# Optimization experiments

Hardware: AMD Instinct MI355X
Metric: run time of the kernel (lower is better)

The kernel has to match this reference:

```python
import jax, jax.numpy as jnp
import numpy as np

HEADS, DIM_HEAD, K_NN, EMB = 4, 64, 16, 256
INNER = HEADS * DIM_HEAD  # 256
POS_HID = 64
ATTN_HID = 4 * DIM_HEAD  # per-head hidden of grouped 1x1 conv MLP


def setup_inputs() -> dict:
    key = jax.random.key(0)
    ks = jax.random.split(key, 16)
    b, n = 2, 4096
    s = 0.05
    inp = {
        "x": jax.random.normal(ks[0], (b, n, EMB), jnp.float32),
        "mask": jnp.ones((b, n), dtype=bool),
        "pos": jax.random.normal(ks[1], (b, n, 3), jnp.float32),
        # to_qkv (no bias)
        "Wqkv": jax.random.normal(ks[2], (EMB, 3 * INNER), jnp.float32) * s,
        # pos_mlp: Linear(3,64) -> ReLU -> Linear(64, inner)
        "Wp1": jax.random.normal(ks[3], (3, POS_HID), jnp.float32) * s,
        "bp1": jax.random.normal(ks[4], (POS_HID,), jnp.float32) * s,
        "Wp2": jax.random.normal(ks[5], (POS_HID, INNER), jnp.float32) * s,
        "bp2": jax.random.normal(ks[6], (INNER,), jnp.float32) * s,
        # attn_mlp: grouped 1x1 convs == per-head linears [h, d_in, d_out]
        "Wa1": jax.random.normal(ks[7], (HEADS, DIM_HEAD, ATTN_HID), jnp.float32) * s,
        "ba1": jax.random.normal(ks[8], (HEADS, ATTN_HID), jnp.float32) * s,
        "Wa2": jax.random.normal(ks[9], (HEADS, ATTN_HID, DIM_HEAD), jnp.float32) * s,
        "ba2": jax.random.normal(ks[10], (HEADS, DIM_HEAD), jnp.float32) * s,
        # to_out
        "Wo": jax.random.normal(ks[11], (INNER, EMB), jnp.float32) * s,
        "bo": jax.random.normal(ks[12], (EMB,), jnp.float32) * s,
    }
    return inp


def reference(x, mask, pos, Wqkv, Wp1, bp1, Wp2, bp2, Wa1, ba1, Wa2, ba2, Wo, bo):
    b, n, _ = x.shape
    h, dh = HEADS, DIM_HEAD

    qkv = x @ Wqkv                              # [b, n, 3*inner]
    q, k, v = jnp.split(qkv, 3, axis=-1)
    to_heads = lambda t: t.reshape(b, n, h, dh).transpose(0, 2, 1, 3)  # [b,h,n,d]
    q, k, v = to_heads(q), to_heads(k), to_heads(v)

    # kNN on pos (per batch, squared euclidean, includes self)
    sq = jnp.sum(pos * pos, axis=-1)
    d2 = sq[:, :, None] + sq[:, None, :] - 2.0 * jnp.einsum('bid,bjd->bij', pos, pos)
    idx = jax.lax.top_k(-d2, K_NN)[1]            # [b, n, K]

    gat_h = jax.vmap(lambda t, i: t[:, i])       # [h,n,d],[n,K] -> [h,n,K,d]
    gat = jax.vmap(lambda t, i: t[i])            # [n,c],[n,K]  -> [n,K,c]

    qg = gat_h(q, idx)                           # [b,h,n,K,d]
    kg = gat_h(k, idx)
    vg = gat_h(v, idx)

    rel = gat(pos, idx) - pos[:, :, None, :]     # [b,n,K,3]
    rpe = jax.nn.relu(rel @ Wp1 + bp1) @ Wp2 + bp2               # [b,n,K,inner]
    rpe = rpe.reshape(b, n, K_NN, h, dh).transpose(0, 3, 1, 2, 4)  # [b,h,n,K,d]

    attn_in = qg - kg + rpe                      # [b,h,n,K,d]
    hid = jax.nn.relu(jnp.einsum('bhnkd,hde->bhnke', attn_in, Wa1)
                      + ba1[None, :, None, None, :])
    sim = (jnp.einsum('bhnke,hed->bhnkd', hid, Wa2)
           + ba2[None, :, None, None, :])        # [b,h,n,K,d]

    mg = jax.vmap(lambda m, i: m[i])(mask, idx)  # [b,n,K]
    pair = (mask[:, :, None] & mg)[:, None, :, :, None]
    sim = jnp.where(pair, sim, -jnp.finfo(sim.dtype).max)

    attn = jax.nn.softmax(sim, axis=3)           # over neighbors j
    # F.normalize over dim=-2 of [b,(h d),i,j] == over the point axis i
    attn = attn / jnp.maximum(jnp.linalg.norm(attn, axis=2, keepdims=True), 1e-12)

    agg = jnp.sum(attn * (vg + rpe), axis=3)     # [b,h,n,d]
    agg = agg.transpose(0, 2, 1, 3).reshape(b, n, h * dh)
    return agg @ Wo + bo
```

## Files before the change

### kernel.cpp

```cpp
#include <hip/hip_runtime.h>
#include <float.h>

typedef unsigned int uint;
typedef unsigned short ushort;

typedef _Float16 f16x8 __attribute__((ext_vector_type(8)));
typedef float f32x4 __attribute__((ext_vector_type(4)));
#define MFMA_F16(A, B, C) __builtin_amdgcn_mfma_f32_16x16x32_f16(A, B, C, 0, 0, 0)

__device__ __forceinline__ ushort f2h(float f) {
    _Float16 h = (_Float16)f;
    return __builtin_bit_cast(ushort, h);
}
__device__ __forceinline__ float h2f(ushort u) {
    _Float16 h = __builtin_bit_cast(_Float16, u);
    return (float)h;
}
__device__ __forceinline__ uint pack2(float a, float b) {
    return (uint)f2h(a) | ((uint)f2h(b) << 16);
}
__device__ __forceinline__ uint pkrtz(float a, float b) {
    return __builtin_bit_cast(uint, __builtin_amdgcn_cvt_pkrtz(a, b));
}
__device__ __forceinline__ f16x8 cast8(uint4 u) {
    return __builtin_bit_cast(f16x8, u);
}

template <int CTRL>
__device__ __forceinline__ void dpp_min(float& v, int& j) {
    int vp = __builtin_amdgcn_update_dpp(__float_as_int(v), __float_as_int(v),
                                         CTRL, 0xF, 0xF, false);
    int jp = __builtin_amdgcn_update_dpp(j, j, CTRL, 0xF, 0xF, false);
    float vf = __int_as_float(vp);
    bool better = (vf < v) || (vf == v && jp < j);
    v = better ? vf : v;
    j = better ? jp : j;
}
__device__ __forceinline__ void wave_min(float& v, int& j) {
    dpp_min<0x121>(v, j);
    dpp_min<0x122>(v, j);
    dpp_min<0x124>(v, j);
    dpp_min<0x128>(v, j);
    float ov = __shfl_xor(v, 16);
    int oj = __shfl_xor(j, 16);
    bool better = (ov < v) || (ov == v && oj < j);
    v = better ? ov : v;
    j = better ? oj : j;
    ov = __shfl_xor(v, 32);
    oj = __shfl_xor(j, 32);
    better = (ov < v) || (ov == v && oj < j);
    v = better ? ov : v;
    j = better ? oj : j;
}

__global__ void prep_kernel(const float* __restrict__ Wqkv, const float* __restrict__ Wa1,
                            const float* __restrict__ Wa2, const float* __restrict__ Wo,
                            const float* __restrict__ Wp2, const float* __restrict__ ba1,
                            ushort* __restrict__ WcatT, ushort* __restrict__ Wa1T,
                            ushort* __restrict__ Wa2T, ushort* __restrict__ WoT,
                            ushort* __restrict__ Wp2T, ushort* __restrict__ ba1p) {
    int t = blockIdx.x * 256 + threadIdx.x;
    {
        int cc2 = t >> 8, kk = t & 255;
        float val;
        if (cc2 < 256) val = Wqkv[kk * 768 + cc2] - Wqkv[kk * 768 + 256 + cc2];
        else           val = Wqkv[kk * 768 + 256 + cc2];
        WcatT[t] = f2h(val);
    }
    if (t < 65536) {
        int hh = t >> 14, r = t & 16383;
        int e = r >> 6, kin = r & 63;
        Wa1T[t] = f2h(Wa1[((size_t)(hh * 64 + kin)) * 256 + e]);
        int d = r >> 8, pos = r & 255;
        int ec = pos >> 5, lg = (pos >> 3) & 3, q = pos & 7;
        int e2 = ec * 32 + ((q >> 2) & 1) * 16 + lg * 4 + (q & 3);
        Wa2T[t] = f2h(Wa2[((size_t)(hh * 256 + e2)) * 64 + d]);
        int c3 = t >> 8, k3 = t & 255;
        WoT[t] = f2h(Wo[k3 * 256 + c3]);
    }
    if (t < 16384) {
        int row = t >> 6, p = t & 63;
        int h = row >> 6, s = row & 63;
        int ct = s >> 4, rr = s & 15;
        int d = (ct >> 1) * 32 + ((rr >> 2) & 3) * 8 + (ct & 1) * 4 + (rr & 3);
        Wp2T[t] = f2h(Wp2[p * 256 + h * 64 + d]);
    }
    if (t < 1024) {
        int h = t >> 8, pos = t & 255;
        int ec = pos >> 5, lg = (pos >> 3) & 3, q = pos & 7;
        int e2 = ec * 32 + ((q >> 2) & 1) * 16 + lg * 4 + (q & 3);
        ba1p[t] = f2h(ba1[h * 256 + e2]);
    }
}

__global__ void pos4_kernel(const float* __restrict__ pos, float4* __restrict__ pos4) {
    int t = blockIdx.x * 256 + threadIdx.x;
    float x = pos[t * 3 + 0], y = pos[t * 3 + 1], z = pos[t * 3 + 2];
    float4 o = {x, y, z, x * x + y * y + z * z};
    pos4[t] = o;
}

template <int MODE>
__global__ __launch_bounds__(256)
void hgemm(const void* __restrict__ Av, const ushort* __restrict__ Bt,
           const float* __restrict__ bias, void* __restrict__ C0v, ushort* __restrict__ C1h) {
    __shared__ ushort Af[64 * 40];
    __shared__ ushort Bf[128 * 40];
    const int tid = threadIdx.x;
    const int l = tid & 63, wv = tid >> 6;
    const int lg = l >> 4, lr = l & 15;
    const int row0 = blockIdx.x * 64, col0 = blockIdx.y * 128;
    const int mrow = (wv >> 1) * 32, ncol = (wv & 1) * 64;
    f32x4 acc[2][4];
#pragma unroll
    for (int mt = 0; mt < 2; ++mt)
#pragma unroll
        for (int nt = 0; nt < 4; ++nt) acc[mt][nt] = (f32x4){0.f, 0.f, 0.f, 0.f};

    for (int kk = 0; kk < 256; kk += 32) {
        if (MODE == 0) {
            const float* A = (const float*)Av;
            int r = tid >> 2, kq = (tid & 3) * 8;
            float4 a0 = *(const float4*)&A[(size_t)(row0 + r) * 256 + kk + kq];
            float4 a1 = *(const float4*)&A[(size_t)(row0 + r) * 256 + kk + kq + 4];
            uint4 u;
            u.x = pack2(a0.x, a0.y); u.y = pack2(a0.z, a0.w);
            u.z = pack2(a1.x, a1.y); u.w = pack2(a1.z, a1.w);
            *(uint4*)&Af[r * 40 + kq] = u;
        } else {
            const ushort* Ah = (const ushort*)Av;
            int r = tid >> 2, kq = (tid & 3) * 8;
            *(uint4*)&Af[r * 40 + kq] = *(const uint4*)&Ah[(size_t)(row0 + r) * 256 + kk + kq];
        }
        {
            int r = tid >> 1, hh = (tid & 1) * 16;
            const uint4* src = (const uint4*)&Bt[(size_t)(col0 + r) * 256 + kk + hh];
            uint4 b0 = src[0], b1 = src[1];
            *(uint4*)&Bf[r * 40 + hh] = b0;
            *(uint4*)&Bf[r * 40 + hh + 8] = b1;
        }
        __syncthreads();
        f16x8 afr[2], bfr[4];
#pragma unroll
        for (int mt = 0; mt < 2; ++mt)
            afr[mt] = *(const f16x8*)&Af[(mrow + mt * 16 + lr) * 40 + lg * 8];
#pragma unroll
        for (int nt = 0; nt < 4; ++nt)
            bfr[nt] = *(const f16x8*)&Bf[(ncol + nt * 16 + lr) * 40 + lg * 8];
#pragma unroll
        for (int mt = 0; mt < 2; ++mt)
#pragma unroll
            for (int nt = 0; nt < 4; ++nt)
                acc[mt][nt] = MFMA_F16(afr[mt], bfr[nt], acc[mt][nt]);
        __syncthreads();
    }
#pragma unroll
    for (int mt = 0; mt < 2; ++mt)
#pragma unroll
        for (int nt = 0; nt < 4; ++nt)
#pragma unroll
            for (int j = 0; j < 4; ++j) {
                int m = row0 + mrow + mt * 16 + lg * 4 + j;
                int n = col0 + ncol + nt * 16 + lr;
                float v = acc[mt][nt][j];
                if (MODE == 1) {
                    ((float*)C0v)[(size_t)m * 256 + n] = v + bias[n];
                } else {
                    int b = m >> 12, i2 = m & 4095;
                    if (n < 256) {
                        int hh = n >> 6, d = n & 63;
                        ((ushort*)C0v)[((size_t)((b * 4 + hh) << 12) + i2) * 64 + d] = f2h(v);
                    } else {
                        int n2 = n - 256;
                        int hh = n2 >> 6, d = n2 & 63;
                        C1h[((size_t)((b * 4 + hh) << 12) + i2) * 64 + d] = f2h(v);
                    }
                }
            }
}

__global__ __launch_bounds__(256, 6)
void knn_kernel(const float4* __restrict__ pos4, int* __restrict__ idx_out) {
    const int tid = threadIdx.x;
    const int lane = tid & 63, wv = tid >> 6;
    const int pblk = blockIdx.x;
    const int b = pblk >> 10;
    const int i = ((pblk & 1023) << 2) + wv;
    const float4* p4 = pos4 + (size_t)b * 4096;
    float4 pi = p4[i];
    float xi = pi.x, yi = pi.y, zi = pi.z, sqi = pi.w;
    const int SENT = 0x7fffffff;

    float v1[4], v2[4];
    int j1[4], j2[4];
#pragma unroll
    for (int g = 0; g < 4; ++g) { v1[g] = FLT_MAX; v2[g] = FLT_MAX; j1[g] = SENT; j2[g] = SENT; }
#pragma unroll 4
    for (int m = 0; m < 64; ++m) {
        int j = m * 64 + lane;
        float4 pj = p4[j];
        float v = sqi + pj.w - 2.f * (xi * pj.x + yi * pj.y + zi * pj.z);
        int g = m & 3;
        bool bb1 = (v < v1[g]) || (v == v1[g] && j < j1[g]);
        bool bb2 = (v < v2[g]) || (v == v2[g] && j < j2[g]);
        float nv2 = bb1 ? v1[g] : (bb2 ? v : v2[g]);
        int   nj2 = bb1 ? j1[g] : (bb2 ? j : j2[g]);
        v1[g] = bb1 ? v : v1[g];
        j1[g] = bb1 ? j : j1[g];
        v2[g] = nv2;
        j2[g] = nj2;
    }
    auto mergef = [](float& a1, int& aj1, float& a2, int& aj2,
                     float b1v, int bj1, float b2v, int bj2) {
        bool aFirst = (a1 < b1v) || (a1 == b1v && aj1 < bj1);
        float r1 = aFirst ? a1 : b1v;
        int rj1 = aFirst ? aj1 : bj1;
        float cand = aFirst ? a2 : b2v;
        int candj = aFirst ? aj2 : bj2;
        float oth = aFirst ? b1v : a1;
        int othj = aFirst ? bj1 : aj1;
        bool second = (cand < oth) || (cand == oth && candj < othj);
        a1 = r1; aj1 = rj1;
        a2 = second ? cand : oth;
        aj2 = second ? candj : othj;
    };
    mergef(v1[0], j1[0], v2[0], j2[0], v1[1], j1[1], v2[1], j2[1]);
    mergef(v1[2], j1[2], v2[2], j2[2], v1[3], j1[3], v2[3], j2[3]);
    mergef(v1[0], j1[0], v2[0], j2[0], v1[2], j1[2], v2[2], j2[2]);
    float c1v = v1[0], c2v = v2[0];
    int c1j = j1[0], c2j = j2[0];

    unsigned long long extr = 0ull;
    int keep = 0;
#pragma unroll 1
    for (int r = 0; r < 16; ++r) {
        float bv = c1v;
        int bj = c1j;
        wave_min(bv, bj);
        if (lane == r) keep = bj;
        int c = bj & 63;
        if (lane == (bj >> 6)) extr |= (1ull << c);
        if (lane == c) {
            c1v = c2v; c1j = c2j;
            c2v = FLT_MAX; c2j = SENT;
        }
        unsigned long long need = __ballot(lane == c && c1j == SENT);
        if (need) {
            int j = lane * 64 + c;
            float4 pj = p4[j];
            float v = sqi + pj.w - 2.f * (xi * pj.x + yi * pj.y + zi * pj.z);
            bool dead = (((extr >> c) & 1ull) != 0ull);
            v = dead ? FLT_MAX : v;
            float w1 = v; int wj1 = j;
            wave_min(w1, wj1);
            float w2 = (j == wj1) ? FLT_MAX : v;
            int wj2 = (j == wj1) ? SENT : j;
            wave_min(w2, wj2);
            if (lane == c) { c1v = w1; c1j = wj1; c2v = w2; c2j = wj2; }
        }
    }
    if (lane < 16)
        idx_out[((size_t)b * 4096 + i) * 16 + lane] = keep;
}

__global__ __launch_bounds__(256)
void attn_mfma(const ushort* __restrict__ qmkh, const ushort* __restrict__ vbufh,
               const float4* __restrict__ pos4, const int* __restrict__ idxb,
               const ushort* __restrict__ Wa1Tg, const ushort* __restrict__ Wa2Tg,
               const ushort* __restrict__ Wp2Tg, const ushort* __restrict__ ba1p,
               const float* __restrict__ ba2,
               const float* __restrict__ Wp1, const float* __restrict__ bp1,
               const float* __restrict__ bp2,
               ushort* __restrict__ prodbuf, float* __restrict__ part) {
    __shared__ ushort W1[256 * 72];
    __shared__ ushort W2[64 * 264];
    __shared__ ushort scr[4][16 * 88];
    const int tid = threadIdx.x;
    const int l = tid & 63, wv = tid >> 6;
    const int lg = l >> 4, lr = l & 15;
    const int c = blockIdx.x;
    const int h = c >> 8, rc = c & 255, b = rc >> 7, chunk = rc & 127;
    const int bh = b * 4 + h;

    {
        const uint4* g1 = (const uint4*)(Wa1Tg + (size_t)h * 16384);
        const uint4* g2 = (const uint4*)(Wa2Tg + (size_t)h * 16384);
#pragma unroll
        for (int it = 0; it < 8; ++it) {
            int ci = it * 256 + tid;
            *(uint4*)&W1[(ci >> 3) * 72 + (ci & 7) * 8] = g1[ci];
        }
#pragma unroll
        for (int it = 0; it < 8; ++it) {
            int ci = it * 256 + tid;
            *(uint4*)&W2[(ci >> 5) * 264 + (ci & 31) * 8] = g2[ci];
        }
    }
    __syncthreads();

    float b2v[4];
#pragma unroll
    for (int dt = 0; dt < 4; ++dt) b2v[dt] = ba2[h * 64 + dt * 16 + lr];

    f16x8 wp2f[4][2];
#pragma unroll
    for (int ct = 0; ct < 4; ++ct)
#pragma unroll
        for (int kt = 0; kt < 2; ++kt)
            wp2f[ct][kt] = *(const f16x8*)&Wp2Tg[(size_t)(h * 64 + ct * 16 + lr) * 64 + kt * 32 + lg * 8];
    f16x8 wp1h[3][2], bp1h[2], bp2h[2];
#pragma unroll
    for (int cc = 0; cc < 3; ++cc)
#pragma unroll
        for (int kt = 0; kt < 2; ++kt) {
            float4 w0 = *(const float4*)&Wp1[cc * 64 + kt * 32 + lg * 8];
            float4 w1 = *(const float4*)&Wp1[cc * 64 + kt * 32 + lg * 8 + 4];
            f16x8 wv8;
            wv8[0] = (_Float16)w0.x; wv8[1] = (_Float16)w0.y;
            wv8[2] = (_Float16)w0.z; wv8[3] = (_Float16)w0.w;
            wv8[4] = (_Float16)w1.x; wv8[5] = (_Float16)w1.y;
            wv8[6] = (_Float16)w1.z; wv8[7] = (_Float16)w1.w;
            wp1h[cc][kt] = wv8;
        }
#pragma unroll
    for (int kt = 0; kt < 2; ++kt) {
        float4 b0 = *(const float4*)&bp1[kt * 32 + lg * 8];
        float4 b1 = *(const float4*)&bp1[kt * 32 + lg * 8 + 4];
        f16x8 bv8;
        bv8[0] = (_Float16)b0.x; bv8[1] = (_Float16)b0.y;
        bv8[2] = (_Float16)b0.z; bv8[3] = (_Float16)b0.w;
        bv8[4] = (_Float16)b1.x; bv8[5] = (_Float16)b1.y;
        bv8[6] = (_Float16)b1.z; bv8[7] = (_Float16)b1.w;
        bp1h[kt] = bv8;
        float4 c0 = *(const float4*)&bp2[h * 64 + kt * 32 + lg * 8];
        float4 c1 = *(const float4*)&bp2[h * 64 + kt * 32 + lg * 8 + 4];
        f16x8 cv8;
        cv8[0] = (_Float16)c0.x; cv8[1] = (_Float16)c0.y;
        cv8[2] = (_Float16)c0.z; cv8[3] = (_Float16)c0.w;
        cv8[4] = (_Float16)c1.x; cv8[5] = (_Float16)c1.y;
        cv8[6] = (_Float16)c1.z; cv8[7] = (_Float16)c1.w;
        bp2h[kt] = cv8;
    }
    const float4* pb4 = pos4 + (size_t)b * 4096;
    const ushort* qbase = qmkh + (size_t)bh * 4096 * 64;
    const ushort* vbase = vbufh + (size_t)bh * 4096 * 64;
    const ushort* b1base = ba1p + h * 256;
    ushort* sw = &scr[wv][0];

    float asq[4][4];
#pragma unroll
    for (int dt = 0; dt < 4; ++dt)
#pragma unroll
        for (int j2 = 0; j2 < 4; ++j2) asq[dt][j2] = 0.f;

    for (int pg = 0; pg < 2; ++pg) {
        const int i0 = chunk * 32 + pg * 16 + wv * 4;
        int jj[4];
        f16x8 ain[4][2], rpef[4][2];
#pragma unroll
        for (int pp = 0; pp < 4; ++pp) {
            int i = i0 + pp;
            int row = ((b << 12) + i) * 16 + lr;
            int j = idxb[row];
            jj[pp] = j;
            float4 pj = pb4[j];
            float4 pi = pb4[i];
            _Float16 rxh = (_Float16)(pj.x - pi.x);
            _Float16 ryh = (_Float16)(pj.y - pi.y);
            _Float16 rzh = (_Float16)(pj.z - pi.z);
            f16x8 hf[2];
#pragma unroll
            for (int kt = 0; kt < 2; ++kt) {
                f16x8 t = bp1h[kt] + rxh * wp1h[0][kt] + ryh * wp1h[1][kt] + rzh * wp1h[2][kt];
#pragma unroll
                for (int q = 0; q < 8; ++q) t[q] = t[q] > (_Float16)0.f ? t[q] : (_Float16)0.f;
                hf[kt] = t;
            }
            f32x4 z4 = {0.f, 0.f, 0.f, 0.f};
            f32x4 racc[4];
#pragma unroll
            for (int ct = 0; ct < 4; ++ct) {
                racc[ct] = MFMA_F16(wp2f[ct][0], hf[0], z4);
                racc[ct] = MFMA_F16(wp2f[ct][1], hf[1], racc[ct]);
            }
            const ushort* qb = qbase + ((size_t)j) * 64 + lg * 8;
#pragma unroll
            for (int kt = 0; kt < 2; ++kt) {
                uint4 rp;
                rp.x = pkrtz(racc[2 * kt][0], racc[2 * kt][1]);
                rp.y = pkrtz(racc[2 * kt][2], racc[2 * kt][3]);
                rp.z = pkrtz(racc[2 * kt + 1][0], racc[2 * kt + 1][1]);
                rp.w = pkrtz(racc[2 * kt + 1][2], racc[2 * kt + 1][3]);
                f16x8 rv = cast8(rp) + bp2h[kt];
                rpef[pp][kt] = rv;
                f16x8 qv = *(const f16x8*)(qb + kt * 32);
                ain[pp][kt] = qv + rv;
            }
        }
        f32x4 acc[4][4];
#pragma unroll
        for (int pp = 0; pp < 4; ++pp)
#pragma unroll
            for (int dt = 0; dt < 4; ++dt) acc[pp][dt] = (f32x4){0.f, 0.f, 0.f, 0.f};

        for (int ec = 0; ec < 8; ++ec) {
            f16x8 A1[2][2], B2f[4];
#pragma unroll
            for (int et = 0; et < 2; ++et)
#pragma unroll
                for (int kt = 0; kt < 2; ++kt)
                    A1[et][kt] = *(const f16x8*)&W1[(ec * 32 + et * 16 + lr) * 72 + kt * 32 + lg * 8];
#pragma unroll
            for (int dt = 0; dt < 4; ++dt)
                B2f[dt] = *(const f16x8*)&W2[(dt * 16 + lr) * 264 + ec * 32 + lg * 8];
            f16x8 b1h = *(const f16x8*)&b1base[ec * 32 + lg * 8];
#pragma unroll
            for (int pp = 0; pp < 4; ++pp) {
                f32x4 z = {0.f, 0.f, 0.f, 0.f};
                f32x4 h0 = MFMA_F16(A1[0][0], ain[pp][0], z);
                h0 = MFMA_F16(A1[0][1], ain[pp][1], h0);
                f32x4 h1 = MFMA_F16(A1[1][0], ain[pp][0], z);
                h1 = MFMA_F16(A1[1][1], ain[pp][1], h1);
                uint4 hp;
                hp.x = pkrtz(h0[0], h0[1]); hp.y = pkrtz(h0[2], h0[3]);
                hp.z = pkrtz(h1[0], h1[1]); hp.w = pkrtz(h1[2], h1[3]);
                f16x8 hv = cast8(hp) + b1h;
#pragma unroll
                for (int q = 0; q < 8; ++q) hv[q] = hv[q] > (_Float16)0.f ? hv[q] : (_Float16)0.f;
#pragma unroll
                for (int dt = 0; dt < 4; ++dt)
                    acc[pp][dt] = MFMA_F16(hv, B2f[dt], acc[pp][dt]);
            }
        }
#pragma unroll
        for (int pp = 0; pp < 4; ++pp) {
            int i = i0 + pp;
            float at[4][4];
#pragma unroll
            for (int dt = 0; dt < 4; ++dt) {
                float v0 = acc[pp][dt][0] + b2v[dt];
                float v1 = acc[pp][dt][1] + b2v[dt];
                float v2 = acc[pp][dt][2] + b2v[dt];
                float v3 = acc[pp][dt][3] + b2v[dt];
                float m = fmaxf(fmaxf(v0, v1), fmaxf(v2, v3));
                m = fmaxf(m, __shfl_xor(m, 16));
                m = fmaxf(m, __shfl_xor(m, 32));
                float e0 = __expf(v0 - m), e1 = __expf(v1 - m);
                float e2 = __expf(v2 - m), e3 = __expf(v3 - m);
                float s = e0 + e1 + e2 + e3;
                s += __shfl_xor(s, 16);
                s += __shfl_xor(s, 32);
                float is = 1.f / s;
                at[dt][0] = e0 * is; at[dt][1] = e1 * is;
                at[dt][2] = e2 * is; at[dt][3] = e3 * is;
                asq[dt][0] += at[dt][0] * at[dt][0];
                asq[dt][1] += at[dt][1] * at[dt][1];
                asq[dt][2] += at[dt][2] * at[dt][2];
                asq[dt][3] += at[dt][3] * at[dt][3];
            }
#pragma unroll
            for (int dt = 0; dt < 4; ++dt) {
                sw[(lg * 4 + 0) * 88 + dt * 16 + lr] = f2h(at[dt][0]);
                sw[(lg * 4 + 1) * 88 + dt * 16 + lr] = f2h(at[dt][1]);
                sw[(lg * 4 + 2) * 88 + dt * 16 + lr] = f2h(at[dt][2]);
                sw[(lg * 4 + 3) * 88 + dt * 16 + lr] = f2h(at[dt][3]);
            }
            const ushort* vb = vbase + (size_t)jj[pp] * 64 + lg * 8;
            ushort* pr = prodbuf + ((size_t)(bh * 4096 + i) * 16 + lr) * 64 + lg * 8;
#pragma unroll
            for (int kt = 0; kt < 2; ++kt) {
                f16x8 atB = *(const f16x8*)&sw[lr * 88 + kt * 32 + lg * 8];
                f16x8 vv = *(const f16x8*)(vb + kt * 32);
                f16x8 p = (vv + rpef[pp][kt]) * atB;
                *(f16x8*)(pr + kt * 32) = p;
            }
        }
    }
    float* scrF = (float*)&scr[0][0];
#pragma unroll
    for (int dt = 0; dt < 4; ++dt) {
        __syncthreads();
#pragma unroll
        for (int j2 = 0; j2 < 4; ++j2)
            scrF[wv * 288 + lr * 18 + lg * 4 + j2] = asq[dt][j2];
        __syncthreads();
        int fr = tid >> 4, fk = tid & 15;
        float s = scrF[fr * 18 + fk] + scrF[288 + fr * 18 + fk] +
                  scrF[576 + fr * 18 + fk] + scrF[864 + fr * 18 + fk];
        part[((size_t)c * 4 + dt) * 256 + tid] = s;
    }
}

__global__ void inv_kernel(const float* __restrict__ part, float* __restrict__ invn) {
    int t = blockIdx.x * 256 + threadIdx.x;
    int bh = t >> 10, f = t & 1023;
    int d = f >> 4, k = f & 15;
    int dt = d >> 4, lr = d & 15;
    int cbase = (bh & 3) * 256 + (bh >> 2) * 128;
    float s = 0.f;
    for (int cc = 0; cc < 128; ++cc)
        s += part[((size_t)(cbase + cc) * 4 + dt) * 256 + lr * 16 + k];
    invn[t] = 1.f / fmaxf(sqrtf(s), 1e-12f);
}

__global__ void finalize_kernel(const ushort* __restrict__ prodbuf, const float* __restrict__ invn,
                                ushort* __restrict__ aggh) {
    int t = blockIdx.x * 256 + threadIdx.x;
    int d = t & 63;
    int i = (t >> 6) & 4095;
    int bh = t >> 18;
    const ushort* pr = prodbuf + ((size_t)(bh * 4096 + i)) * 1024 + d;
    const float* iv = invn + bh * 1024 + d * 16;
    float accv = 0.f;
#pragma unroll
    for (int k = 0; k < 16; ++k)
        accv += h2f(pr[(size_t)k * 64]) * iv[k];
    int hh = bh & 3, bb = bh >> 2;
    aggh[((size_t)(bb * 4096 + i)) * 256 + hh * 64 + d] = f2h(accv);
}

extern "C" void kernel_launch(void* const* d_in, const int* in_sizes, int n_in,
                              void* d_out, int out_size, void* d_ws, size_t ws_size,
                              hipStream_t stream) {
    const float* x    = (const float*)d_in[0];
    const float* pos  = (const float*)d_in[2];
    const float* Wqkv = (const float*)d_in[3];
    const float* Wp1  = (const float*)d_in[4];
    const float* bp1  = (const float*)d_in[5];
    const float* Wp2  = (const float*)d_in[6];
    const float* bp2  = (const float*)d_in[7];
    const float* Wa1  = (const float*)d_in[8];
    const float* ba1  = (const float*)d_in[9];
    const float* Wa2  = (const float*)d_in[10];
    const float* ba2  = (const float*)d_in[11];
    const float* Wo   = (const float*)d_in[12];
    const float* bo   = (const float*)d_in[13];

    char* base = (char*)d_ws;
    size_t off = 0;
    auto carve = [&](size_t bytes) -> char* {
        char* r = base + off;
        off = (off + bytes + 255) & ~(size_t)255;
        return r;
    };
    ushort* qmkh   = (ushort*)carve(4194304);
    ushort* vbufh  = (ushort*)carve(4194304);
    ushort* WcatT  = (ushort*)carve(262144);
    ushort* Wa1Tg  = (ushort*)carve(131072);
    ushort* Wa2Tg  = (ushort*)carve(131072);
    ushort* WoT    = (ushort*)carve(131072);
    ushort* Wp2Tg  = (ushort*)carve(32768);
    ushort* ba1pg  = (ushort*)carve(2048);
    float4* pos4   = (float4*)carve(131072);
    int*    idx    = (int*)carve(524288);
    ushort* prodbuf= (ushort*)carve(67108864);
    float*  part   = (float*)carve(4194304);
    float*  invn   = (float*)carve(32768);
    ushort* aggh   = (ushort*)carve(4194304);

    prep_kernel<<<512, 256, 0, stream>>>(Wqkv, Wa1, Wa2, Wo, Wp2, ba1,
                                         WcatT, Wa1Tg, Wa2Tg, WoT, Wp2Tg, ba1pg);
    pos4_kernel<<<32, 256, 0, stream>>>(pos, pos4);
    hgemm<0><<<dim3(128, 4), 256, 0, stream>>>(x, WcatT, nullptr, qmkh, vbufh);
    knn_kernel<<<2048, 256, 0, stream>>>(pos4, idx);
    attn_mfma<<<1024, 256, 0, stream>>>(qmkh, vbufh, pos4, idx, Wa1Tg, Wa2Tg, Wp2Tg, ba1pg,
                                        ba2, Wp1, bp1, bp2, prodbuf, part);
    inv_kernel<<<32, 256, 0, stream>>>(part, invn);
    finalize_kernel<<<8192, 256, 0, stream>>>(prodbuf, invn, aggh);
    hgemm<1><<<dim3(128, 2), 256, 0, stream>>>(aggh, WoT, bo, d_out, nullptr);
}
```

Baseline: 190.8 us.

## Raise attn_mfma occupancy by shrinking per-wave work, LDS and register footprint

The attention kernel now handles 2 points per wave per pass instead of 4 and launches twice as many blocks. It drops the W1 LDS copy and the register-resident Wp2 fragments, reading both from global/L1 instead. The rpe values are recomputed in the epilogue rather than kept live across the MLP, and launch bounds request 4 blocks per CU. This cuts LDS and VGPR pressure to raise occupancy, at the cost of redundant rpe MFMA work, more global weight loads, and a larger partial-sum reduction in inv_kernel.

```diff
diff --git a/kernel.cpp b/kernel.cpp
--- a/kernel.cpp
+++ b/kernel.cpp
@@ -263,7 +263,7 @@
         idx_out[((size_t)b * 4096 + i) * 16 + lane] = keep;
 }
 
-__global__ __launch_bounds__(256)
+__global__ __launch_bounds__(256, 4)
 void attn_mfma(const ushort* __restrict__ qmkh, const ushort* __restrict__ vbufh,
                const float4* __restrict__ pos4, const int* __restrict__ idxb,
                const ushort* __restrict__ Wa1Tg, const ushort* __restrict__ Wa2Tg,
@@ -272,24 +272,17 @@
                const float* __restrict__ Wp1, const float* __restrict__ bp1,
                const float* __restrict__ bp2,
                ushort* __restrict__ prodbuf, float* __restrict__ part) {
-    __shared__ ushort W1[256 * 72];
     __shared__ ushort W2[64 * 264];
     __shared__ ushort scr[4][16 * 88];
     const int tid = threadIdx.x;
     const int l = tid & 63, wv = tid >> 6;
     const int lg = l >> 4, lr = l & 15;
     const int c = blockIdx.x;
-    const int h = c >> 8, rc = c & 255, b = rc >> 7, chunk = rc & 127;
+    const int h = c >> 9, rc = c & 511, b = rc >> 8, chunk = rc & 255;
     const int bh = b * 4 + h;
 
     {
-        const uint4* g1 = (const uint4*)(Wa1Tg + (size_t)h * 16384);
         const uint4* g2 = (const uint4*)(Wa2Tg + (size_t)h * 16384);
-#pragma unroll
-        for (int it = 0; it < 8; ++it) {
-            int ci = it * 256 + tid;
-            *(uint4*)&W1[(ci >> 3) * 72 + (ci & 7) * 8] = g1[ci];
-        }
 #pragma unroll
         for (int it = 0; it < 8; ++it) {
             int ci = it * 256 + tid;
@@ -298,16 +291,13 @@
     }
     __syncthreads();
 
+    const ushort* w1g = Wa1Tg + (size_t)h * 16384;
+    const ushort* wp2g = Wp2Tg + (size_t)h * 64 * 64;
+
     float b2v[4];
 #pragma unroll
     for (int dt = 0; dt < 4; ++dt) b2v[dt] = ba2[h * 64 + dt * 16 + lr];
 
-    f16x8 wp2f[4][2];
-#pragma unroll
-    for (int ct = 0; ct < 4; ++ct)
-#pragma unroll
-        for (int kt = 0; kt < 2; ++kt)
-            wp2f[ct][kt] = *(const f16x8*)&Wp2Tg[(size_t)(h * 64 + ct * 16 + lr) * 64 + kt * 32 + lg * 8];
     f16x8 wp1h[3][2], bp1h[2], bp2h[2];
 #pragma unroll
     for (int cc = 0; cc < 3; ++cc)
@@ -347,6 +337,36 @@
     const ushort* b1base = ba1p + h * 256;
     ushort* sw = &scr[wv][0];
 
+    auto rpe_of = [&](const f16x8 hf[2], f16x8 rv[2]) {
+        f32x4 z4 = {0.f, 0.f, 0.f, 0.f};
+        f32x4 racc[4];
+#pragma unroll
+        for (int ct = 0; ct < 4; ++ct) {
+            f16x8 wp0 = *(const f16x8*)&wp2g[(size_t)(ct * 16 + lr) * 64 + lg * 8];
+            f16x8 wp1 = *(const f16x8*)&wp2g[(size_t)(ct * 16 + lr) * 64 + 32 + lg * 8];
+            racc[ct] = MFMA_F16(wp0, hf[0], z4);
+            racc[ct] = MFMA_F16(wp1, hf[1], racc[ct]);
+        }
+#pragma unroll
+        for (int kt = 0; kt < 2; ++kt) {
+            uint4 rp;
+            rp.x = pkrtz(racc[2 * kt][0], racc[2 * kt][1]);
+            rp.y = pkrtz(racc[2 * kt][2], racc[2 * kt][3]);
+            rp.z = pkrtz(racc[2 * kt + 1][0], racc[2 * kt + 1][1]);
+            rp.w = pkrtz(racc[2 * kt + 1][2], racc[2 * kt + 1][3]);
+            rv[kt] = cast8(rp) + bp2h[kt];
+        }
+    };
+    auto hf_of = [&](_Float16 rxh, _Float16 ryh, _Float16 rzh, f16x8 hf[2]) {
+#pragma unroll
+        for (int kt = 0; kt < 2; ++kt) {
+            f16x8 t = bp1h[kt] + rxh * wp1h[0][kt] + ryh * wp1h[1][kt] + rzh * wp1h[2][kt];
+#pragma unroll
+            for (int q = 0; q < 8; ++q) t[q] = t[q] > (_Float16)0.f ? t[q] : (_Float16)0.f;
+            hf[kt] = t;
+        }
+    };
+
     float asq[4][4];
 #pragma unroll
     for (int dt = 0; dt < 4; ++dt)
@@ -354,11 +374,12 @@
         for (int j2 = 0; j2 < 4; ++j2) asq[dt][j2] = 0.f;
 
     for (int pg = 0; pg < 2; ++pg) {
-        const int i0 = chunk * 32 + pg * 16 + wv * 4;
-        int jj[4];
-        f16x8 ain[4][2], rpef[4][2];
-#pragma unroll
-        for (int pp = 0; pp < 4; ++pp) {
+        const int i0 = chunk * 16 + pg * 8 + wv * 2;
+        int jj[2];
+        _Float16 rxs[2], rys[2], rzs[2];
+        f16x8 ain[2][2];
+#pragma unroll
+        for (int pp = 0; pp < 2; ++pp) {
             int i = i0 + pp;
             int row = ((b << 12) + i) * 16 + lr;
             int j = idxb[row];
@@ -368,38 +389,20 @@
             _Float16 rxh = (_Float16)(pj.x - pi.x);
             _Float16 ryh = (_Float16)(pj.y - pi.y);
             _Float16 rzh = (_Float16)(pj.z - pi.z);
-            f16x8 hf[2];
+            rxs[pp] = rxh; rys[pp] = ryh; rzs[pp] = rzh;
+            f16x8 hf[2], rv[2];
+            hf_of(rxh, ryh, rzh, hf);
+            rpe_of(hf, rv);
+            const ushort* qb = qbase + ((size_t)j) * 64 + lg * 8;
 #pragma unroll
             for (int kt = 0; kt < 2; ++kt) {
-                f16x8 t = bp1h[kt] + rxh * wp1h[0][kt] + ryh * wp1h[1][kt] + rzh * wp1h[2][kt];
-#pragma unroll
-                for (int q = 0; q < 8; ++q) t[q] = t[q] > (_Float16)0.f ? t[q] : (_Float16)0.f;
-                hf[kt] = t;
+                f16x8 qv = *(const f16x8*)(qb + kt * 32);
+                ain[pp][kt] = qv + rv[kt];
             }
-            f32x4 z4 = {0.f, 0.f, 0.f, 0.f};
-            f32x4 racc[4];
-#pragma unroll
-            for (int ct = 0; ct < 4; ++ct) {
-                racc[ct] = MFMA_F16(wp2f[ct][0], hf[0], z4);
-                racc[ct] = MFMA_F16(wp2f[ct][1], hf[1], racc[ct]);
-            }
-            const ushort* qb = qbase + ((size_t)j) * 64 + lg * 8;
-#pragma unroll
-            for (int kt = 0; kt < 2; ++kt) {
-                uint4 rp;
-                rp.x = pkrtz(racc[2 * kt][0], racc[2 * kt][1]);
-                rp.y = pkrtz(racc[2 * kt][2], racc[2 * kt][3]);
-                rp.z = pkrtz(racc[2 * kt + 1][0], racc[2 * kt + 1][1]);
-                rp.w = pkrtz(racc[2 * kt + 1][2], racc[2 * kt + 1][3]);
-                f16x8 rv = cast8(rp) + bp2h[kt];
-                rpef[pp][kt] = rv;
-                f16x8 qv = *(const f16x8*)(qb + kt * 32);
-                ain[pp][kt] = qv + rv;
-            }
-        }
-        f32x4 acc[4][4];
-#pragma unroll
-        for (int pp = 0; pp < 4; ++pp)
+        }
+        f32x4 acc[2][4];
+#pragma unroll
+        for (int pp = 0; pp < 2; ++pp)
 #pragma unroll
             for (int dt = 0; dt < 4; ++dt) acc[pp][dt] = (f32x4){0.f, 0.f, 0.f, 0.f};
 
@@ -409,13 +412,13 @@
             for (int et = 0; et < 2; ++et)
 #pragma unroll
                 for (int kt = 0; kt < 2; ++kt)
-                    A1[et][kt] = *(const f16x8*)&W1[(ec * 32 + et * 16 + lr) * 72 + kt * 32 + lg * 8];
+                    A1[et][kt] = *(const f16x8*)&w1g[(size_t)(ec * 32 + et * 16 + lr) * 64 + kt * 32 + lg * 8];
 #pragma unroll
             for (int dt = 0; dt < 4; ++dt)
                 B2f[dt] = *(const f16x8*)&W2[(dt * 16 + lr) * 264 + ec * 32 + lg * 8];
             f16x8 b1h = *(const f16x8*)&b1base[ec * 32 + lg * 8];
 #pragma unroll
-            for (int pp = 0; pp < 4; ++pp) {
+            for (int pp = 0; pp < 2; ++pp) {
                 f32x4 z = {0.f, 0.f, 0.f, 0.f};
                 f32x4 h0 = MFMA_F16(A1[0][0], ain[pp][0], z);
                 h0 = MFMA_F16(A1[0][1], ain[pp][1], h0);
@@ -433,7 +436,7 @@
             }
         }
 #pragma unroll
-        for (int pp = 0; pp < 4; ++pp) {
+        for (int pp = 0; pp < 2; ++pp) {
             int i = i0 + pp;
             float at[4][4];
 #pragma unroll
@@ -458,6 +461,9 @@
                 asq[dt][2] += at[dt][2] * at[dt][2];
                 asq[dt][3] += at[dt][3] * at[dt][3];
             }
+            f16x8 hf[2], rv[2];
+            hf_of(rxs[pp], rys[pp], rzs[pp], hf);
+            rpe_of(hf, rv);
 #pragma unroll
             for (int dt = 0; dt < 4; ++dt) {
                 sw[(lg * 4 + 0) * 88 + dt * 16 + lr] = f2h(at[dt][0]);
@@ -471,7 +477,7 @@
             for (int kt = 0; kt < 2; ++kt) {
                 f16x8 atB = *(const f16x8*)&sw[lr * 88 + kt * 32 + lg * 8];
                 f16x8 vv = *(const f16x8*)(vb + kt * 32);
-                f16x8 p = (vv + rpef[pp][kt]) * atB;
+                f16x8 p = (vv + rv[kt]) * atB;
                 *(f16x8*)(pr + kt * 32) = p;
             }
         }
@@ -496,9 +502,9 @@
     int bh = t >> 10, f = t & 1023;
     int d = f >> 4, k = f & 15;
     int dt = d >> 4, lr = d & 15;
-    int cbase = (bh & 3) * 256 + (bh >> 2) * 128;
+    int cbase = (bh & 3) * 512 + (bh >> 2) * 256;
     float s = 0.f;
-    for (int cc = 0; cc < 128; ++cc)
+    for (int cc = 0; cc < 256; ++cc)
         s += part[((size_t)(cbase + cc) * 4 + dt) * 256 + lr * 16 + k];
     invn[t] = 1.f / fmaxf(sqrtf(s), 1e-12f);
 }
@@ -554,7 +560,7 @@
     float4* pos4   = (float4*)carve(131072);
     int*    idx    = (int*)carve(524288);
     ushort* prodbuf= (ushort*)carve(67108864);
-    float*  part   = (float*)carve(4194304);
+    float*  part   = (float*)carve(8388608);
     float*  invn   = (float*)carve(32768);
     ushort* aggh   = (ushort*)carve(4194304);
 
@@ -563,7 +569,7 @@
     pos4_kernel<<<32, 256, 0, stream>>>(pos, pos4);
     hgemm<0><<<dim3(128, 4), 256, 0, stream>>>(x, WcatT, nullptr, qmkh, vbufh);
     knn_kernel<<<2048, 256, 0, stream>>>(pos4, idx);
-    attn_mfma<<<1024, 256, 0, stream>>>(qmkh, vbufh, pos4, idx, Wa1Tg, Wa2Tg, Wp2Tg, ba1pg,
+    attn_mfma<<<2048, 256, 0, stream>>>(qmkh, vbufh, pos4, idx, Wa1Tg, Wa2Tg, Wp2Tg, ba1pg,
                                         ba2, Wp1, bp1, bp2, prodbuf, part);
     inv_kernel<<<32, 256, 0, stream>>>(part, invn);
     finalize_kernel<<<8192, 256, 0, stream>>>(prodbuf, invn, aggh);
```

Measured after the change: 254.4 us. +33.3%, slower.
